# Optimization experiments

Measured on AMD Instinct MI355X. Metric: run time of the kernel, lower is better.

## Reference

```python
import jax, jax.numpy as jnp
import numpy as np

NUM_M = 2_000_000
NUM_T = 512
N = 16
NUM_GEN = N * (N - 1) // 2  # 120
NUM_STEPS = 64
TAU = 1.0


def _make_bases():
    # skew-symmetric so(n) basis, matching the torch buffer construction order
    bases = np.zeros((NUM_GEN, N, N), np.float32)
    k = 0
    for i in range(N):
        for j in range(i + 1, N):
            bases[k, i, j] = -1.0
            bases[k, j, i] = 1.0
            k += 1
    return jnp.asarray(bases)


def setup_inputs() -> dict:
    key = jax.random.key(0)
    ks = jax.random.split(key, 8)
    W = jax.random.normal(ks[0], (NUM_M, N), jnp.float32)
    emb_weight = W / jnp.linalg.norm(W, axis=-1, keepdims=True)  # normalized at init
    transition_coeffs = jax.random.normal(ks[1], (NUM_T, NUM_GEN), jnp.float32) * 0.1

    def lin(k, fi, fo):  # torch nn.Linear default init
        bound = 1.0 / np.sqrt(fi)
        kw, kb = jax.random.split(k)
        w = jax.random.uniform(kw, (fi, fo), jnp.float32, -bound, bound)
        b = jax.random.uniform(kb, (fo,), jnp.float32, -bound, bound)
        return w, b

    w1, b1 = lin(ks[2], 2 * N, 256)
    w2, b2 = lin(ks[3], 256, 128)
    w3, b3 = lin(ks[4], 128, NUM_T)

    v_src = jax.random.uniform(ks[5], (1, NUM_M), jnp.float32)
    v_target = jax.random.uniform(ks[6], (1, NUM_M), jnp.float32)
    # pre-sampled Gumbel(0,1) noise for gumbel_softmax, one draw per step
    u = jax.random.uniform(ks[7], (NUM_STEPS, 1, NUM_T), jnp.float32, 1e-6, 1.0 - 1e-6)
    gumbel = -jnp.log(-jnp.log(u))

    return {
        'v_src': v_src, 'v_target': v_target,
        'emb_weight': emb_weight, 'transition_coeffs': transition_coeffs,
        'bases': _make_bases(),
        'w1': w1, 'b1': b1, 'w2': w2, 'b2': b2, 'w3': w3, 'b3': b3,
        'gumbel': gumbel, 'num_steps': NUM_STEPS,
    }


def reference(v_src, v_target, emb_weight, transition_coeffs, bases,
              w1, b1, w2, b2, w3, b3, gumbel, num_steps):
    # training=True path of PetriNetAlignmentPredictor.forward, tau=1.0
    embs = emb_weight / jnp.linalg.norm(emb_weight, axis=-1, keepdims=True)
    v_cur = v_src @ embs      # [1, n]  (memory-bound matvec over num_m)
    v_tgt = v_target @ embs   # [1, n]
    gens = jnp.einsum('tg,gnm->tnm', transition_coeffs, bases)  # [num_t, n, n]
    expm_b = jax.vmap(jax.scipy.linalg.expm)

    def step(v, g):
        h = jax.nn.relu(jnp.concatenate([v, v_tgt], axis=-1) @ w1 + b1)
        h = jax.nn.relu(h @ w2 + b2)
        logits = h @ w3 + b3                       # [1, num_t]
        # gumbel_softmax(hard=True) with straight-through estimator
        y = jax.nn.softmax((logits + g) / TAU, axis=-1)
        hard = jax.nn.one_hot(jnp.argmax(y, axis=-1), logits.shape[-1], dtype=y.dtype)
        one_hot = hard + y - jax.lax.stop_gradient(y)
        omega = jnp.einsum('bt,tnm->bnm', one_hot, gens)  # skew-symmetric [1, n, n]
        R = expm_b(omega)
        v2 = jnp.einsum('bnm,bm->bn', R, v)
        v2 = v2 / jnp.linalg.norm(v2, axis=-1, keepdims=True)
        return v2, logits

    v_fin, logits_seq = jax.lax.scan(step, v_cur, gumbel[:num_steps])
    pred_marking = jax.nn.softmax(v_fin @ embs.T, axis=-1)  # [1, num_m]
    return pred_marking, logits_seq[:, 0, :]  # squeeze batch dim -> [num_steps, num_t]
```

## Files before the change

### kernel.cpp

```cpp
#include <hip/hip_runtime.h>

#define M_TOTAL   2000000
#define NT        512
#define K1_BLOCKS 2048

__device__ __forceinline__ float rlf(float v, int l) {
    union { float f; int i; } u; u.f = v;
    u.i = __builtin_amdgcn_readlane(u.i, l);
    return u.f;
}

__device__ __forceinline__ void bar_lds() {
    asm volatile("s_waitcnt lgkmcnt(0)" ::: "memory");
    __builtin_amdgcn_s_barrier();
    asm volatile("" ::: "memory");
}

#define REP16(M)  M(0) M(1) M(2) M(3) M(4) M(5) M(6) M(7) M(8) M(9) M(10) M(11) M(12) M(13) M(14) M(15)
#define REP16B(M) M(16) M(17) M(18) M(19) M(20) M(21) M(22) M(23) M(24) M(25) M(26) M(27) M(28) M(29) M(30) M(31)

#define VLD4(dst, base, c) { const volatile float* _p = (base) + 4*(c); \
    dst.x = _p[0]; dst.y = _p[1]; dst.z = _p[2]; dst.w = _p[3]; }

extern "C" __global__ __launch_bounds__(256)
void k_reduce(const float* __restrict__ emb, const float* __restrict__ vsrc,
              const float* __restrict__ vtgt, double* __restrict__ partials)
{
    const int tid = threadIdx.x;
    const int bid = blockIdx.x;
    const int q = tid & 3;
    double aS[4], aT[4];
#pragma unroll
    for (int i = 0; i < 4; i++) { aS[i] = 0.0; aT[i] = 0.0; }

    const float4* emb4 = (const float4*)emb;
    for (long long f = (long long)bid * 256 + tid; f < (long long)M_TOTAL * 4;
         f += (long long)K1_BLOCKS * 256) {
        float4 e = emb4[f];
        long long r = f >> 2;
        float sq = fmaf(e.x, e.x, fmaf(e.y, e.y, fmaf(e.z, e.z, e.w * e.w)));
        sq += __shfl_xor(sq, 1);
        sq += __shfl_xor(sq, 2);
        float invn = 1.0f / sqrtf(sq);
        float s = vsrc[r] * invn;
        float t = vtgt[r] * invn;
        aS[0] += (double)(s * e.x); aS[1] += (double)(s * e.y);
        aS[2] += (double)(s * e.z); aS[3] += (double)(s * e.w);
        aT[0] += (double)(t * e.x); aT[1] += (double)(t * e.y);
        aT[2] += (double)(t * e.z); aT[3] += (double)(t * e.w);
    }
#pragma unroll
    for (int i = 0; i < 4; i++) {
#pragma unroll
        for (int off = 32; off >= 4; off >>= 1) {
            aS[i] += __shfl_down(aS[i], off);
            aT[i] += __shfl_down(aT[i], off);
        }
    }
    __shared__ double lred[4][32];
    int lane = tid & 63, wv = tid >> 6;
    if (lane < 4) {
#pragma unroll
        for (int i = 0; i < 4; i++) {
            lred[wv][lane * 4 + i]      = aS[i];
            lred[wv][16 + lane * 4 + i] = aT[i];
        }
    }
    __syncthreads();
    if (tid < 32) {
        double v = lred[0][tid] + lred[1][tid] + lred[2][tid] + lred[3][tid];
        partials[(long long)bid * 32 + tid] = v;
    }
    (void)q;
}

extern "C" __global__ __launch_bounds__(256)
void k_expm(const float* __restrict__ tc, float* __restrict__ Rtab)
{
    const int b = blockIdx.x;
    const int t = threadIdx.x;
    const int i = t >> 4, j = t & 15;
    __shared__ float Om[256];
    __shared__ float Ms[256];

    const float* crow = tc + b * 120;
    float o = 0.0f;
    if (i < j)      o = -crow[(i * (31 - i)) / 2 + (j - i - 1)];
    else if (i > j) o =  crow[(j * (31 - j)) / 2 + (i - j - 1)];
    Om[t] = o;
    Ms[t] = o;
    float s = (i == j ? 1.0f : 0.0f) + o;
    __syncthreads();

#pragma unroll
    for (int k = 2; k <= 16; k++) {
        float a0 = 0.0f, a1 = 0.0f, a2 = 0.0f, a3 = 0.0f;
#pragma unroll
        for (int m = 0; m < 4; m++) {
            a0 = fmaf(Om[i * 16 + m],      Ms[m * 16 + j],        a0);
            a1 = fmaf(Om[i * 16 + 4 + m],  Ms[(4 + m) * 16 + j],  a1);
            a2 = fmaf(Om[i * 16 + 8 + m],  Ms[(8 + m) * 16 + j],  a2);
            a3 = fmaf(Om[i * 16 + 12 + m], Ms[(12 + m) * 16 + j], a3);
        }
        float acc = ((a0 + a1) + (a2 + a3)) * (1.0f / (float)k);
        __syncthreads();
        Ms[t] = acc;
        s += acc;
        __syncthreads();
    }
    Rtab[b * 256 + t] = s;
}

extern "C" __global__ __launch_bounds__(128)
void k_prep(const float* __restrict__ w2g, const float* __restrict__ w3g,
            float* __restrict__ w2R, float* __restrict__ w3R)
{
    const int b = blockIdx.x, k = threadIdx.x;
    if (b < 512) {
        w3R[b * 128 + k] = w3g[k * 512 + b];
    } else {
        const int p2 = b - 512;
        const int j2 = k;
        for (int m = 0; m < 64; m++)
            w2R[(((p2 << 7) | j2) * 64) + m] = w2g[(64 * p2 + m) * 128 + j2];
    }
}

extern "C" __global__ __launch_bounds__(512)
__attribute__((amdgpu_waves_per_eu(2, 2)))
void k_steps(const double* __restrict__ partials,
             const float* __restrict__ w1g, const float* __restrict__ b1g,
             const float* __restrict__ b2g, const float* __restrict__ b3g,
             const float* __restrict__ w2R, const float* __restrict__ w3R,
             const float* __restrict__ Rtab, const float* __restrict__ gum,
             const int* __restrict__ nsp,
             float* __restrict__ outL, float* __restrict__ vf_out)
{
    __shared__ float h1s[256];
    __shared__ float h2p[512];
    __shared__ float xs[32];
    __shared__ float b2s[128];
    __shared__ float rkeys[8];
    __shared__ int   ridx[8];

    const int t = threadIdx.x;
    const int lane = t & 63;
    const int wv = t >> 6;
    const int j2 = t & 127, p2 = t >> 7;
    const int c1 = t & 255;

    const volatile float* w3v = (const volatile float*)(w3R + (size_t)t * 128);
    const volatile float* w2v = (const volatile float*)(w2R + (size_t)t * 64);
#define W3D(c) float4 w3_##c; VLD4(w3_##c, w3v, c)
    REP16(W3D) REP16B(W3D)
#undef W3D
#define W2D(c) float4 w2_##c; VLD4(w2_##c, w2v, c)
    REP16(W2D)
#undef W2D
    const float b3r = b3g[t];

    float w1r[16];
    {
        const volatile float* w1v = (const volatile float*)w1g;
#pragma unroll
        for (int m = 0; m < 16; m++) w1r[m] = w1v[m * 256 + c1];
    }
    if (t < 128) b2s[t] = b2g[t];

    float warm = 0.0f;
    for (int i = t; i < 512 * 256 / 4; i += 512) {
        float4 rv = ((const float4*)Rtab)[i];
        warm += (rv.x + rv.y) + (rv.z + rv.w);
    }

    {
        int c = t >> 4, r = t & 15;
        double v = 0.0;
        for (int k = r; k < K1_BLOCKS; k += 16) v += partials[k * 32 + c];
        v += __shfl_xor(v, 1); v += __shfl_xor(v, 2);
        v += __shfl_xor(v, 4); v += __shfl_xor(v, 8);
        if (r == 0) xs[c] = (float)v;
    }

    int ns = nsp[0];
    if (ns > 64) ns = 64;
    if (ns < 0)  ns = 0;
    if (ns == -2147483647) vf_out[0] = warm;

    __syncthreads();

    float b1e;
    {
        float a = b1g[c1];
#pragma unroll
        for (int m = 0; m < 16; m++)
            a = fmaf(xs[16 + m], w1g[(16 + m) * 256 + c1], a);
        b1e = a;
    }
    float vreg = xs[lane & 15];

    if (ns == 0 && t < 16) vf_out[t] = xs[t];

    const int i16 = lane & 15, q4 = lane >> 4;

    for (int step = 0; step < ns; step++) {
        float gv = gum[step * 512 + t];

        if (t < 256) {
            float a0 = 0.0f, a1 = 0.0f;
#pragma unroll
            for (int m = 0; m < 8; m++) {
                a0 = fmaf(rlf(vreg, m),     w1r[m],     a0);
                a1 = fmaf(rlf(vreg, 8 + m), w1r[8 + m], a1);
            }
            h1s[t] = fmaxf((a0 + a1) + b1e, 0.0f);
        }
        bar_lds();

        {
            float h1seg = h1s[(p2 << 6) | lane];
            float a0 = 0.0f, a1 = 0.0f, a2 = 0.0f, a3 = 0.0f;
#define L2C(c) { a0 = fmaf(rlf(h1seg, 4*(c)+0), w2_##c.x, a0); \
                 a1 = fmaf(rlf(h1seg, 4*(c)+1), w2_##c.y, a1); \
                 a2 = fmaf(rlf(h1seg, 4*(c)+2), w2_##c.z, a2); \
                 a3 = fmaf(rlf(h1seg, 4*(c)+3), w2_##c.w, a3); }
            REP16(L2C)
#undef L2C
            h2p[(p2 << 7) | j2] = (a0 + a1) + (a2 + a3);
        }
        bar_lds();

        float lg;
        {
            float h2lo = fmaxf(((h2p[lane] + h2p[128 + lane]) +
                                (h2p[256 + lane] + h2p[384 + lane])) + b2s[lane], 0.0f);
            float h2hi = fmaxf(((h2p[64 + lane] + h2p[192 + lane]) +
                                (h2p[320 + lane] + h2p[448 + lane])) + b2s[64 + lane], 0.0f);
            float lg0 = 0.0f, lg1 = 0.0f, lg2 = 0.0f, lg3 = 0.0f;
#define L3LO(c) { lg0 = fmaf(rlf(h2lo, 4*(c)+0), w3_##c.x, lg0); \
                  lg1 = fmaf(rlf(h2lo, 4*(c)+1), w3_##c.y, lg1); \
                  lg2 = fmaf(rlf(h2lo, 4*(c)+2), w3_##c.z, lg2); \
                  lg3 = fmaf(rlf(h2lo, 4*(c)+3), w3_##c.w, lg3); }
#define L3HI(c) { lg0 = fmaf(rlf(h2hi, 4*(c)-64), w3_##c.x, lg0); \
                  lg1 = fmaf(rlf(h2hi, 4*(c)-63), w3_##c.y, lg1); \
                  lg2 = fmaf(rlf(h2hi, 4*(c)-62), w3_##c.z, lg2); \
                  lg3 = fmaf(rlf(h2hi, 4*(c)-61), w3_##c.w, lg3); }
            REP16(L3LO) REP16B(L3HI)
#undef L3LO
#undef L3HI
            lg = ((lg0 + lg1) + (lg2 + lg3)) + b3r;
        }

        {
            float key = lg + gv;
            int   idx = t;
#pragma unroll
            for (int off = 32; off; off >>= 1) {
                float ok = __shfl_down(key, off);
                int   oi = __shfl_down(idx, off);
                if (ok > key || (ok == key && oi < idx)) { key = ok; idx = oi; }
            }
            if (lane == 0) { rkeys[wv] = key; ridx[wv] = idx; }
        }
        bar_lds();

        outL[step * 512 + t] = lg;

        {
            float bk = rkeys[0]; int bi = ridx[0];
#pragma unroll
            for (int w = 1; w < 8; w++) {
                float ok = rkeys[w]; int oi = ridx[w];
                if (ok > bk || (ok == bk && oi < bi)) { bk = ok; bi = oi; }
            }
            const float4 rr = *(const float4*)(Rtab + bi * 256 + i16 * 16 + 4 * q4);
            float rw0 = __shfl(vreg, 20 * q4 + 0);
            float rw1 = __shfl(vreg, 20 * q4 + 1);
            float rw2 = __shfl(vreg, 20 * q4 + 2);
            float rw3 = __shfl(vreg, 20 * q4 + 3);
            float pr = rr.x * rw0;
            pr = fmaf(rr.y, rw1, pr);
            pr = fmaf(rr.z, rw2, pr);
            pr = fmaf(rr.w, rw3, pr);
            pr += __shfl_xor(pr, 16);
            pr += __shfl_xor(pr, 32);
            float n2 = pr * pr;
            n2 += __shfl_xor(n2, 1);
            n2 += __shfl_xor(n2, 2);
            n2 += __shfl_xor(n2, 4);
            n2 += __shfl_xor(n2, 8);
            float invn = 1.0f / sqrtf(n2);
            vreg = pr * invn;
            if (step == ns - 1 && t < 16) vf_out[t] = vreg;
        }
    }
}

extern "C" __global__ __launch_bounds__(256)
void k_scores(const float* __restrict__ emb, const float* __restrict__ vf16,
              float* __restrict__ outP, double* __restrict__ sums)
{
    __shared__ float vfs[16];
    const int tid = threadIdx.x;
    const int bid = blockIdx.x;
    const int q = tid & 3;
    if (tid < 16) vfs[tid] = vf16[tid];
    __syncthreads();
    float v0 = vfs[q * 4 + 0], v1 = vfs[q * 4 + 1], v2 = vfs[q * 4 + 2], v3 = vfs[q * 4 + 3];

    const float4* emb4 = (const float4*)emb;
    double bsum = 0.0;
    for (long long f = (long long)bid * 256 + tid; f < (long long)M_TOTAL * 4;
         f += (long long)K1_BLOCKS * 256) {
        float4 e = emb4[f];
        long long r = f >> 2;
        float sq = fmaf(e.x, e.x, fmaf(e.y, e.y, fmaf(e.z, e.z, e.w * e.w)));
        float d  = fmaf(e.x, v0, fmaf(e.y, v1, fmaf(e.z, v2, e.w * v3)));
        sq += __shfl_xor(sq, 1);  d += __shfl_xor(d, 1);
        sq += __shfl_xor(sq, 2);  d += __shfl_xor(d, 2);
        float ex = expf(d / sqrtf(sq));
        if (q == 0) {
            outP[r] = ex;
            bsum += (double)ex;
        }
    }
#pragma unroll
    for (int off = 4; off <= 32; off <<= 1) bsum += __shfl_down(bsum, off);
    __shared__ double lred[4];
    if ((tid & 63) == 0) lred[tid >> 6] = bsum;
    __syncthreads();
    if (tid == 0) sums[bid] = lred[0] + lred[1] + lred[2] + lred[3];
}

extern "C" __global__ __launch_bounds__(256)
void k_total(const double* __restrict__ sums, double* __restrict__ invp)
{
    const int tid = threadIdx.x;
    double v = 0.0;
    for (int k = tid; k < K1_BLOCKS; k += 256) v += sums[k];
#pragma unroll
    for (int off = 32; off; off >>= 1) v += __shfl_down(v, off);
    __shared__ double lred[4];
    if ((tid & 63) == 0) lred[tid >> 6] = v;
    __syncthreads();
    if (tid == 0) invp[0] = 1.0 / (lred[0] + lred[1] + lred[2] + lred[3]);
}

extern "C" __global__ __launch_bounds__(256)
void k_scale(float* __restrict__ outP, const double* __restrict__ invp)
{
    const float inv = (float)invp[0];
    long long r4 = (long long)blockIdx.x * 256 + threadIdx.x;
    if (r4 < M_TOTAL / 4) {
        float4* p = (float4*)outP;
        float4 v = p[r4];
        v.x *= inv; v.y *= inv; v.z *= inv; v.w *= inv;
        p[r4] = v;
    }
}

extern "C" void kernel_launch(void* const* d_in, const int* in_sizes, int n_in,
                              void* d_out, int out_size, void* d_ws, size_t ws_size,
                              hipStream_t stream)
{
    const float* vsrc = (const float*)d_in[0];
    const float* vtgt = (const float*)d_in[1];
    const float* emb  = (const float*)d_in[2];
    const float* tc   = (const float*)d_in[3];
    const float* w1 = (const float*)d_in[5];
    const float* b1 = (const float*)d_in[6];
    const float* w2 = (const float*)d_in[7];
    const float* b2 = (const float*)d_in[8];
    const float* w3 = (const float*)d_in[9];
    const float* b3 = (const float*)d_in[10];
    const float* gum = (const float*)d_in[11];
    const int* nsp   = (const int*)d_in[12];

    float* outP = (float*)d_out;
    float* outL = outP + M_TOTAL;

    double* wsd      = (double*)d_ws;
    double* partials = wsd;
    double* sums     = wsd + K1_BLOCKS * 32;
    double* invp     = sums + K1_BLOCKS;
    float*  vf       = (float*)(invp + 1);

    float* Rtab = outP;
    float* w3R  = outP + 131072;
    float* w2R  = outP + 196608;

    k_expm<<<NT, 256, 0, stream>>>(tc, Rtab);
    k_prep<<<516, 128, 0, stream>>>(w2, w3, w2R, w3R);
    k_reduce<<<K1_BLOCKS, 256, 0, stream>>>(emb, vsrc, vtgt, partials);
    k_steps<<<1, 512, 0, stream>>>(partials, w1, b1, b2, b3, w2R, w3R, Rtab, gum, nsp, outL, vf);
    k_scores<<<K1_BLOCKS, 256, 0, stream>>>(emb, vf, outP, sums);
    k_total<<<1, 256, 0, stream>>>(sums, invp);
    k_scale<<<(M_TOTAL / 4 + 255) / 256, 256, 0, stream>>>(outP, invp);
}
```

Baseline: 552.6 us.

## Split serial MLP steps across 1024 threads with halved per-thread weight slices

Expands the single-block sequential step kernel from 512 to 1024 threads. Each thread now holds half as many w2/w3 weights in registers, and layer-3 partial logits are combined through an added shared-memory stage. w1 moves from registers into LDS, and the weight-repacking kernel is rearranged to match the new slices. The aim is to cut the per-step latency of the 64-step serial chain, at the cost of an extra barrier per step and more LDS traffic.

```diff
diff --git a/kernel.cpp b/kernel.cpp
--- a/kernel.cpp
+++ b/kernel.cpp
@@ -17,7 +17,7 @@
 }
 
 #define REP16(M)  M(0) M(1) M(2) M(3) M(4) M(5) M(6) M(7) M(8) M(9) M(10) M(11) M(12) M(13) M(14) M(15)
-#define REP16B(M) M(16) M(17) M(18) M(19) M(20) M(21) M(22) M(23) M(24) M(25) M(26) M(27) M(28) M(29) M(30) M(31)
+#define REP8(M)   M(0) M(1) M(2) M(3) M(4) M(5) M(6) M(7)
 
 #define VLD4(dst, base, c) { const volatile float* _p = (base) + 4*(c); \
     dst.x = _p[0]; dst.y = _p[1]; dst.z = _p[2]; dst.w = _p[3]; }
@@ -28,7 +28,6 @@
 {
     const int tid = threadIdx.x;
     const int bid = blockIdx.x;
-    const int q = tid & 3;
     double aS[4], aT[4];
 #pragma unroll
     for (int i = 0; i < 4; i++) { aS[i] = 0.0; aT[i] = 0.0; }
@@ -71,7 +70,6 @@
         double v = lred[0][tid] + lred[1][tid] + lred[2][tid] + lred[3][tid];
         partials[(long long)bid * 32 + tid] = v;
     }
-    (void)q;
 }
 
 extern "C" __global__ __launch_bounds__(256)
@@ -111,23 +109,22 @@
     Rtab[b * 256 + t] = s;
 }
 
-extern "C" __global__ __launch_bounds__(128)
+extern "C" __global__ __launch_bounds__(64)
 void k_prep(const float* __restrict__ w2g, const float* __restrict__ w3g,
             float* __restrict__ w2R, float* __restrict__ w3R)
 {
-    const int b = blockIdx.x, k = threadIdx.x;
-    if (b < 512) {
-        w3R[b * 128 + k] = w3g[k * 512 + b];
-    } else {
-        const int p2 = b - 512;
-        const int j2 = k;
-        for (int m = 0; m < 64; m++)
-            w2R[(((p2 << 7) | j2) * 64) + m] = w2g[(64 * p2 + m) * 128 + j2];
-    }
-}
-
-extern "C" __global__ __launch_bounds__(512)
-__attribute__((amdgpu_waves_per_eu(2, 2)))
+    const int b = blockIdx.x;
+    const int l = threadIdx.x;
+    const int o = b & 511, hh = b >> 9;
+    w3R[b * 64 + l] = w3g[(hh * 64 + l) * 512 + o];
+    if (l < 32) {
+        const int p = b >> 7, j = b & 127;
+        w2R[b * 32 + l] = w2g[(p * 32 + l) * 128 + j];
+    }
+}
+
+extern "C" __global__ __launch_bounds__(1024)
+__attribute__((amdgpu_waves_per_eu(4, 4)))
 void k_steps(const double* __restrict__ partials,
              const float* __restrict__ w1g, const float* __restrict__ b1g,
              const float* __restrict__ b2g, const float* __restrict__ b3g,
@@ -136,8 +133,10 @@
              const int* __restrict__ nsp,
              float* __restrict__ outL, float* __restrict__ vf_out)
 {
+    __shared__ float w1s[16 * 256];
     __shared__ float h1s[256];
-    __shared__ float h2p[512];
+    __shared__ float h2p[1024];
+    __shared__ float lgp[1024];
     __shared__ float xs[32];
     __shared__ float b2s[128];
     __shared__ float rkeys[8];
@@ -146,39 +145,33 @@
     const int t = threadIdx.x;
     const int lane = t & 63;
     const int wv = t >> 6;
-    const int j2 = t & 127, p2 = t >> 7;
-    const int c1 = t & 255;
-
-    const volatile float* w3v = (const volatile float*)(w3R + (size_t)t * 128);
-    const volatile float* w2v = (const volatile float*)(w2R + (size_t)t * 64);
+
+    const volatile float* w3v = (const volatile float*)(w3R + (size_t)t * 64);
+    const volatile float* w2v = (const volatile float*)(w2R + (size_t)t * 32);
 #define W3D(c) float4 w3_##c; VLD4(w3_##c, w3v, c)
-    REP16(W3D) REP16B(W3D)
+    REP16(W3D)
 #undef W3D
 #define W2D(c) float4 w2_##c; VLD4(w2_##c, w2v, c)
-    REP16(W2D)
+    REP8(W2D)
 #undef W2D
-    const float b3r = b3g[t];
-
-    float w1r[16];
-    {
-        const volatile float* w1v = (const volatile float*)w1g;
-#pragma unroll
-        for (int m = 0; m < 16; m++) w1r[m] = w1v[m * 256 + c1];
-    }
+    const float b3r = (t < 512) ? b3g[t] : 0.0f;
+
+    for (int i = t; i < 16 * 256; i += 1024) w1s[i] = w1g[i];
     if (t < 128) b2s[t] = b2g[t];
 
     float warm = 0.0f;
-    for (int i = t; i < 512 * 256 / 4; i += 512) {
+    for (int i = t; i < 512 * 256 / 4; i += 1024) {
         float4 rv = ((const float4*)Rtab)[i];
         warm += (rv.x + rv.y) + (rv.z + rv.w);
     }
 
     {
-        int c = t >> 4, r = t & 15;
+        int c = t >> 5, r = t & 31;
         double v = 0.0;
-        for (int k = r; k < K1_BLOCKS; k += 16) v += partials[k * 32 + c];
+        for (int k = r; k < K1_BLOCKS; k += 32) v += partials[k * 32 + c];
         v += __shfl_xor(v, 1); v += __shfl_xor(v, 2);
         v += __shfl_xor(v, 4); v += __shfl_xor(v, 8);
+        v += __shfl_xor(v, 16);
         if (r == 0) xs[c] = (float)v;
     }
 
@@ -189,69 +182,67 @@
 
     __syncthreads();
 
-    float b1e;
-    {
-        float a = b1g[c1];
+    float b1e = 0.0f, vreg = 0.0f;
+    if (t < 256) {
+        float a = b1g[t];
 #pragma unroll
         for (int m = 0; m < 16; m++)
-            a = fmaf(xs[16 + m], w1g[(16 + m) * 256 + c1], a);
+            a = fmaf(xs[16 + m], w1g[(16 + m) * 256 + t], a);
         b1e = a;
-    }
-    float vreg = xs[lane & 15];
+        vreg = xs[lane & 15];
+    }
 
     if (ns == 0 && t < 16) vf_out[t] = xs[t];
 
     const int i16 = lane & 15, q4 = lane >> 4;
 
     for (int step = 0; step < ns; step++) {
-        float gv = gum[step * 512 + t];
+        float gv = (t < 512) ? gum[step * 512 + t] : 0.0f;
 
         if (t < 256) {
             float a0 = 0.0f, a1 = 0.0f;
 #pragma unroll
             for (int m = 0; m < 8; m++) {
-                a0 = fmaf(rlf(vreg, m),     w1r[m],     a0);
-                a1 = fmaf(rlf(vreg, 8 + m), w1r[8 + m], a1);
+                a0 = fmaf(rlf(vreg, m),     w1s[m * 256 + t],       a0);
+                a1 = fmaf(rlf(vreg, 8 + m), w1s[(8 + m) * 256 + t], a1);
             }
             h1s[t] = fmaxf((a0 + a1) + b1e, 0.0f);
         }
         bar_lds();
 
         {
-            float h1seg = h1s[(p2 << 6) | lane];
+            float h1seg = h1s[((t >> 7) << 5) | (lane & 31)];
             float a0 = 0.0f, a1 = 0.0f, a2 = 0.0f, a3 = 0.0f;
 #define L2C(c) { a0 = fmaf(rlf(h1seg, 4*(c)+0), w2_##c.x, a0); \
                  a1 = fmaf(rlf(h1seg, 4*(c)+1), w2_##c.y, a1); \
                  a2 = fmaf(rlf(h1seg, 4*(c)+2), w2_##c.z, a2); \
                  a3 = fmaf(rlf(h1seg, 4*(c)+3), w2_##c.w, a3); }
-            REP16(L2C)
+            REP8(L2C)
 #undef L2C
-            h2p[(p2 << 7) | j2] = (a0 + a1) + (a2 + a3);
+            h2p[t] = (a0 + a1) + (a2 + a3);
         }
         bar_lds();
 
-        float lg;
         {
-            float h2lo = fmaxf(((h2p[lane] + h2p[128 + lane]) +
-                                (h2p[256 + lane] + h2p[384 + lane])) + b2s[lane], 0.0f);
-            float h2hi = fmaxf(((h2p[64 + lane] + h2p[192 + lane]) +
-                                (h2p[320 + lane] + h2p[448 + lane])) + b2s[64 + lane], 0.0f);
+            const int hbl = ((t >> 9) << 6) + lane;
+            float s = b2s[hbl];
+#pragma unroll
+            for (int p = 0; p < 8; p++) s += h2p[p * 128 + hbl];
+            float h2seg = fmaxf(s, 0.0f);
             float lg0 = 0.0f, lg1 = 0.0f, lg2 = 0.0f, lg3 = 0.0f;
-#define L3LO(c) { lg0 = fmaf(rlf(h2lo, 4*(c)+0), w3_##c.x, lg0); \
-                  lg1 = fmaf(rlf(h2lo, 4*(c)+1), w3_##c.y, lg1); \
-                  lg2 = fmaf(rlf(h2lo, 4*(c)+2), w3_##c.z, lg2); \
-                  lg3 = fmaf(rlf(h2lo, 4*(c)+3), w3_##c.w, lg3); }
-#define L3HI(c) { lg0 = fmaf(rlf(h2hi, 4*(c)-64), w3_##c.x, lg0); \
-                  lg1 = fmaf(rlf(h2hi, 4*(c)-63), w3_##c.y, lg1); \
-                  lg2 = fmaf(rlf(h2hi, 4*(c)-62), w3_##c.z, lg2); \
-                  lg3 = fmaf(rlf(h2hi, 4*(c)-61), w3_##c.w, lg3); }
-            REP16(L3LO) REP16B(L3HI)
-#undef L3LO
-#undef L3HI
-            lg = ((lg0 + lg1) + (lg2 + lg3)) + b3r;
-        }
-
-        {
+#define L3C(c) { lg0 = fmaf(rlf(h2seg, 4*(c)+0), w3_##c.x, lg0); \
+                 lg1 = fmaf(rlf(h2seg, 4*(c)+1), w3_##c.y, lg1); \
+                 lg2 = fmaf(rlf(h2seg, 4*(c)+2), w3_##c.z, lg2); \
+                 lg3 = fmaf(rlf(h2seg, 4*(c)+3), w3_##c.w, lg3); }
+            REP16(L3C)
+#undef L3C
+            lgp[t] = (lg0 + lg1) + (lg2 + lg3);
+        }
+        bar_lds();
+
+        if (t < 512) {
+            float lg = (lgp[t] + lgp[512 + t]) + b3r;
+            outL[step * 512 + t] = lg;
             float key = lg + gv;
             int   idx = t;
 #pragma unroll
@@ -264,9 +255,7 @@
         }
         bar_lds();
 
-        outL[step * 512 + t] = lg;
-
-        {
+        if (t < 256) {
             float bk = rkeys[0]; int bi = ridx[0];
 #pragma unroll
             for (int w = 1; w < 8; w++) {
@@ -390,9 +379,9 @@
     float* w2R  = outP + 196608;
 
     k_expm<<<NT, 256, 0, stream>>>(tc, Rtab);
-    k_prep<<<516, 128, 0, stream>>>(w2, w3, w2R, w3R);
+    k_prep<<<1024, 64, 0, stream>>>(w2, w3, w2R, w3R);
     k_reduce<<<K1_BLOCKS, 256, 0, stream>>>(emb, vsrc, vtgt, partials);
-    k_steps<<<1, 512, 0, stream>>>(partials, w1, b1, b2, b3, w2R, w3R, Rtab, gum, nsp, outL, vf);
+    k_steps<<<1, 1024, 0, stream>>>(partials, w1, b1, b2, b3, w2R, w3R, Rtab, gum, nsp, outL, vf);
     k_scores<<<K1_BLOCKS, 256, 0, stream>>>(emb, vf, outP, sums);
     k_total<<<1, 256, 0, stream>>>(sums, invp);
     k_scale<<<(M_TOTAL / 4 + 255) / 256, 256, 0, stream>>>(outP, invp);
```

After: 621.4 us. +12.4%, slower.

## Merge prep kernels, drop total kernel via atomics, and speed step-loop argmax and matvec

Applied to the files above, without the earlier changes.

Fuses k_expm and k_prep into one launch and replaces the k_total kernel with a double atomicAdd into a zeroed accumulator, removing two kernel launches. The partials reduction block count is halved and its final sum is done through shared memory. Inside the serial step loop, argmax now uses DPP max on order-preserving integer keys plus a ballot, and the 16x16 rotation matvec uses one lane per output row with DPP sums. Together these target launch overhead and per-step latency in the single-block loop. The atomic sum changes the floating-point reduction order, so results are no longer deterministic across runs.

```diff
diff --git a/kernel.cpp b/kernel.cpp
--- a/kernel.cpp
+++ b/kernel.cpp
@@ -2,7 +2,8 @@
 
 #define M_TOTAL   2000000
 #define NT        512
-#define K1_BLOCKS 2048
+#define K1_BLOCKS 1024
+#define K3_BLOCKS 2048
 
 __device__ __forceinline__ float rlf(float v, int l) {
     union { float f; int i; } u; u.f = v;
@@ -16,6 +17,21 @@
     asm volatile("" ::: "memory");
 }
 
+#define DPPMAXU(m, ctrl) { unsigned _d = (unsigned)__builtin_amdgcn_update_dpp(0, (int)(m), (ctrl), 0xF, 0xF, true); \
+                           if (_d > (m)) (m) = _d; }
+#define DPPADDF(s, ctrl) { float _d = __int_as_float(__builtin_amdgcn_update_dpp(0, __float_as_int(s), (ctrl), 0xF, 0xF, true)); \
+                           (s) += _d; }
+
+__device__ __forceinline__ unsigned orderf(float f) {
+    unsigned u = __float_as_uint(f);
+    return u ^ (((unsigned)((int)u >> 31)) | 0x80000000u);
+}
+
+__device__ __forceinline__ uint2 pick2(uint2 a, uint2 b) {
+    bool takeb = (b.x > a.x) || (b.x == a.x && b.y < a.y);
+    return takeb ? b : a;
+}
+
 #define REP16(M)  M(0) M(1) M(2) M(3) M(4) M(5) M(6) M(7) M(8) M(9) M(10) M(11) M(12) M(13) M(14) M(15)
 #define REP16B(M) M(16) M(17) M(18) M(19) M(20) M(21) M(22) M(23) M(24) M(25) M(26) M(27) M(28) M(29) M(30) M(31)
 
@@ -28,7 +44,6 @@
 {
     const int tid = threadIdx.x;
     const int bid = blockIdx.x;
-    const int q = tid & 3;
     double aS[4], aT[4];
 #pragma unroll
     for (int i = 0; i < 4; i++) { aS[i] = 0.0; aT[i] = 0.0; }
@@ -71,58 +86,61 @@
         double v = lred[0][tid] + lred[1][tid] + lred[2][tid] + lred[3][tid];
         partials[(long long)bid * 32 + tid] = v;
     }
-    (void)q;
 }
 
 extern "C" __global__ __launch_bounds__(256)
-void k_expm(const float* __restrict__ tc, float* __restrict__ Rtab)
-{
-    const int b = blockIdx.x;
+void k_pre(const float* __restrict__ tc, float* __restrict__ Rtab,
+           const float* __restrict__ w2g, const float* __restrict__ w3g,
+           float* __restrict__ w2R, float* __restrict__ w3R,
+           double* __restrict__ totalp)
+{
+    const int bid = blockIdx.x;
     const int t = threadIdx.x;
-    const int i = t >> 4, j = t & 15;
-    __shared__ float Om[256];
-    __shared__ float Ms[256];
-
-    const float* crow = tc + b * 120;
-    float o = 0.0f;
-    if (i < j)      o = -crow[(i * (31 - i)) / 2 + (j - i - 1)];
-    else if (i > j) o =  crow[(j * (31 - j)) / 2 + (i - j - 1)];
-    Om[t] = o;
-    Ms[t] = o;
-    float s = (i == j ? 1.0f : 0.0f) + o;
-    __syncthreads();
-
-#pragma unroll
-    for (int k = 2; k <= 16; k++) {
-        float a0 = 0.0f, a1 = 0.0f, a2 = 0.0f, a3 = 0.0f;
-#pragma unroll
-        for (int m = 0; m < 4; m++) {
-            a0 = fmaf(Om[i * 16 + m],      Ms[m * 16 + j],        a0);
-            a1 = fmaf(Om[i * 16 + 4 + m],  Ms[(4 + m) * 16 + j],  a1);
-            a2 = fmaf(Om[i * 16 + 8 + m],  Ms[(8 + m) * 16 + j],  a2);
-            a3 = fmaf(Om[i * 16 + 12 + m], Ms[(12 + m) * 16 + j], a3);
-        }
-        float acc = ((a0 + a1) + (a2 + a3)) * (1.0f / (float)k);
+
+    if (bid < 512) {
+        const int i = t >> 4, j = t & 15;
+        __shared__ float Om[256];
+        __shared__ float Ms[256];
+
+        const float* crow = tc + bid * 120;
+        float o = 0.0f;
+        if (i < j)      o = -crow[(i * (31 - i)) / 2 + (j - i - 1)];
+        else if (i > j) o =  crow[(j * (31 - j)) / 2 + (i - j - 1)];
+        Om[t] = o;
+        Ms[t] = o;
+        float s = (i == j ? 1.0f : 0.0f) + o;
         __syncthreads();
-        Ms[t] = acc;
-        s += acc;
-        __syncthreads();
-    }
-    Rtab[b * 256 + t] = s;
-}
-
-extern "C" __global__ __launch_bounds__(128)
-void k_prep(const float* __restrict__ w2g, const float* __restrict__ w3g,
-            float* __restrict__ w2R, float* __restrict__ w3R)
-{
-    const int b = blockIdx.x, k = threadIdx.x;
-    if (b < 512) {
-        w3R[b * 128 + k] = w3g[k * 512 + b];
+
+#pragma unroll
+        for (int k = 2; k <= 16; k++) {
+            float a0 = 0.0f, a1 = 0.0f, a2 = 0.0f, a3 = 0.0f;
+#pragma unroll
+            for (int m = 0; m < 4; m++) {
+                a0 = fmaf(Om[i * 16 + m],      Ms[m * 16 + j],        a0);
+                a1 = fmaf(Om[i * 16 + 4 + m],  Ms[(4 + m) * 16 + j],  a1);
+                a2 = fmaf(Om[i * 16 + 8 + m],  Ms[(8 + m) * 16 + j],  a2);
+                a3 = fmaf(Om[i * 16 + 12 + m], Ms[(12 + m) * 16 + j], a3);
+            }
+            float acc = ((a0 + a1) + (a2 + a3)) * (1.0f / (float)k);
+            __syncthreads();
+            Ms[t] = acc;
+            s += acc;
+            __syncthreads();
+        }
+        Rtab[bid * 256 + t] = s;
     } else {
-        const int p2 = b - 512;
-        const int j2 = k;
-        for (int m = 0; m < 64; m++)
-            w2R[(((p2 << 7) | j2) * 64) + m] = w2g[(64 * p2 + m) * 128 + j2];
+        if (bid == 512 && t == 0) totalp[0] = 0.0;
+        if (t >= 128) return;
+        const int b = bid - 512;
+        const int k = t;
+        if (b < 512) {
+            w3R[b * 128 + k] = w3g[k * 512 + b];
+        } else {
+            const int p2 = b - 512;
+            const int j2 = k;
+            for (int m = 0; m < 64; m++)
+                w2R[(((p2 << 7) | j2) * 64) + m] = w2g[(64 * p2 + m) * 128 + j2];
+        }
     }
 }
 
@@ -140,8 +158,8 @@
     __shared__ float h2p[512];
     __shared__ float xs[32];
     __shared__ float b2s[128];
-    __shared__ float rkeys[8];
-    __shared__ int   ridx[8];
+    __shared__ uint2 kidx[8];
+    __shared__ double dred[512];
 
     const int t = threadIdx.x;
     const int lane = t & 63;
@@ -174,12 +192,10 @@
     }
 
     {
-        int c = t >> 4, r = t & 15;
         double v = 0.0;
-        for (int k = r; k < K1_BLOCKS; k += 16) v += partials[k * 32 + c];
-        v += __shfl_xor(v, 1); v += __shfl_xor(v, 2);
-        v += __shfl_xor(v, 4); v += __shfl_xor(v, 8);
-        if (r == 0) xs[c] = (float)v;
+#pragma unroll 4
+        for (int i = 0; i < (K1_BLOCKS * 32) / 512; i++) v += partials[i * 512 + t];
+        dred[t] = v;
     }
 
     int ns = nsp[0];
@@ -188,20 +204,25 @@
     if (ns == -2147483647) vf_out[0] = warm;
 
     __syncthreads();
-
-    float b1e;
-    {
+    if (t < 32) {
+        double s = 0.0;
+#pragma unroll
+        for (int j = 0; j < 16; j++) s += dred[t + 32 * j];
+        xs[t] = (float)s;
+    }
+    __syncthreads();
+
+    float b1e = 0.0f, vreg = 0.0f;
+    if (t < 256) {
         float a = b1g[c1];
 #pragma unroll
         for (int m = 0; m < 16; m++)
             a = fmaf(xs[16 + m], w1g[(16 + m) * 256 + c1], a);
         b1e = a;
-    }
-    float vreg = xs[lane & 15];
+        vreg = xs[lane & 15];
+    }
 
     if (ns == 0 && t < 16) vf_out[t] = xs[t];
-
-    const int i16 = lane & 15, q4 = lane >> 4;
 
     for (int step = 0; step < ns; step++) {
         float gv = gum[step * 512 + t];
@@ -250,45 +271,63 @@
 #undef L3HI
             lg = ((lg0 + lg1) + (lg2 + lg3)) + b3r;
         }
+        outL[step * 512 + t] = lg;
 
         {
-            float key = lg + gv;
-            int   idx = t;
-#pragma unroll
-            for (int off = 32; off; off >>= 1) {
-                float ok = __shfl_down(key, off);
-                int   oi = __shfl_down(idx, off);
-                if (ok > key || (ok == key && oi < idx)) { key = ok; idx = oi; }
+            unsigned ok = orderf(lg + gv);
+            unsigned m = ok;
+            DPPMAXU(m, 0x111)
+            DPPMAXU(m, 0x112)
+            DPPMAXU(m, 0x114)
+            DPPMAXU(m, 0x118)
+            DPPMAXU(m, 0x142)
+            DPPMAXU(m, 0x143)
+            unsigned wmax = (unsigned)__builtin_amdgcn_readlane((int)m, 63);
+            unsigned long long mask = __ballot(ok == wmax);
+            if (lane == 0) {
+                uint2 kv; kv.x = wmax; kv.y = (unsigned)(wv * 64 + (__ffsll(mask) - 1));
+                kidx[wv] = kv;
             }
-            if (lane == 0) { rkeys[wv] = key; ridx[wv] = idx; }
         }
         bar_lds();
 
-        outL[step * 512 + t] = lg;
-
-        {
-            float bk = rkeys[0]; int bi = ridx[0];
-#pragma unroll
-            for (int w = 1; w < 8; w++) {
-                float ok = rkeys[w]; int oi = ridx[w];
-                if (ok > bk || (ok == bk && oi < bi)) { bk = ok; bi = oi; }
-            }
-            const float4 rr = *(const float4*)(Rtab + bi * 256 + i16 * 16 + 4 * q4);
-            float rw0 = __shfl(vreg, 20 * q4 + 0);
-            float rw1 = __shfl(vreg, 20 * q4 + 1);
-            float rw2 = __shfl(vreg, 20 * q4 + 2);
-            float rw3 = __shfl(vreg, 20 * q4 + 3);
-            float pr = rr.x * rw0;
-            pr = fmaf(rr.y, rw1, pr);
-            pr = fmaf(rr.z, rw2, pr);
-            pr = fmaf(rr.w, rw3, pr);
-            pr += __shfl_xor(pr, 16);
-            pr += __shfl_xor(pr, 32);
-            float n2 = pr * pr;
-            n2 += __shfl_xor(n2, 1);
-            n2 += __shfl_xor(n2, 2);
-            n2 += __shfl_xor(n2, 4);
-            n2 += __shfl_xor(n2, 8);
+        if (t < 256 && lane < 16) {
+            uint2 K0, K1, K2, K3, K4, K5, K6, K7;
+            { uint4 a = *(const uint4*)&kidx[0]; K0.x=a.x; K0.y=a.y; K1.x=a.z; K1.y=a.w; }
+            { uint4 a = *(const uint4*)&kidx[2]; K2.x=a.x; K2.y=a.y; K3.x=a.z; K3.y=a.w; }
+            { uint4 a = *(const uint4*)&kidx[4]; K4.x=a.x; K4.y=a.y; K5.x=a.z; K5.y=a.w; }
+            { uint4 a = *(const uint4*)&kidx[6]; K6.x=a.x; K6.y=a.y; K7.x=a.z; K7.y=a.w; }
+            uint2 w01 = pick2(K0, K1), w23 = pick2(K2, K3);
+            uint2 w45 = pick2(K4, K5), w67 = pick2(K6, K7);
+            uint2 win = pick2(pick2(w01, w23), pick2(w45, w67));
+            const int bi = (int)win.y;
+
+            const float4* rp = (const float4*)(Rtab + (size_t)bi * 256 + lane * 16);
+            float4 ra = rp[0], rb = rp[1], rc = rp[2], rd = rp[3];
+            float pr;
+            pr = ra.x * rlf(vreg, 0);
+            pr = fmaf(ra.y, rlf(vreg, 1), pr);
+            pr = fmaf(ra.z, rlf(vreg, 2), pr);
+            pr = fmaf(ra.w, rlf(vreg, 3), pr);
+            pr = fmaf(rb.x, rlf(vreg, 4), pr);
+            pr = fmaf(rb.y, rlf(vreg, 5), pr);
+            pr = fmaf(rb.z, rlf(vreg, 6), pr);
+            pr = fmaf(rb.w, rlf(vreg, 7), pr);
+            pr = fmaf(rc.x, rlf(vreg, 8), pr);
+            pr = fmaf(rc.y, rlf(vreg, 9), pr);
+            pr = fmaf(rc.z, rlf(vreg, 10), pr);
+            pr = fmaf(rc.w, rlf(vreg, 11), pr);
+            pr = fmaf(rd.x, rlf(vreg, 12), pr);
+            pr = fmaf(rd.y, rlf(vreg, 13), pr);
+            pr = fmaf(rd.z, rlf(vreg, 14), pr);
+            pr = fmaf(rd.w, rlf(vreg, 15), pr);
+
+            float s2 = pr * pr;
+            DPPADDF(s2, 0x111)
+            DPPADDF(s2, 0x112)
+            DPPADDF(s2, 0x114)
+            DPPADDF(s2, 0x118)
+            float n2 = rlf(s2, 15);
             float invn = 1.0f / sqrtf(n2);
             vreg = pr * invn;
             if (step == ns - 1 && t < 16) vf_out[t] = vreg;
@@ -298,7 +337,7 @@
 
 extern "C" __global__ __launch_bounds__(256)
 void k_scores(const float* __restrict__ emb, const float* __restrict__ vf16,
-              float* __restrict__ outP, double* __restrict__ sums)
+              float* __restrict__ outP, double* __restrict__ totalp)
 {
     __shared__ float vfs[16];
     const int tid = threadIdx.x;
@@ -311,7 +350,7 @@
     const float4* emb4 = (const float4*)emb;
     double bsum = 0.0;
     for (long long f = (long long)bid * 256 + tid; f < (long long)M_TOTAL * 4;
-         f += (long long)K1_BLOCKS * 256) {
+         f += (long long)K3_BLOCKS * 256) {
         float4 e = emb4[f];
         long long r = f >> 2;
         float sq = fmaf(e.x, e.x, fmaf(e.y, e.y, fmaf(e.z, e.z, e.w * e.w)));
@@ -329,27 +368,13 @@
     __shared__ double lred[4];
     if ((tid & 63) == 0) lred[tid >> 6] = bsum;
     __syncthreads();
-    if (tid == 0) sums[bid] = lred[0] + lred[1] + lred[2] + lred[3];
+    if (tid == 0) atomicAdd(totalp, lred[0] + lred[1] + lred[2] + lred[3]);
 }
 
 extern "C" __global__ __launch_bounds__(256)
-void k_total(const double* __restrict__ sums, double* __restrict__ invp)
-{
-    const int tid = threadIdx.x;
-    double v = 0.0;
-    for (int k = tid; k < K1_BLOCKS; k += 256) v += sums[k];
-#pragma unroll
-    for (int off = 32; off; off >>= 1) v += __shfl_down(v, off);
-    __shared__ double lred[4];
-    if ((tid & 63) == 0) lred[tid >> 6] = v;
-    __syncthreads();
-    if (tid == 0) invp[0] = 1.0 / (lred[0] + lred[1] + lred[2] + lred[3]);
-}
-
-extern "C" __global__ __launch_bounds__(256)
-void k_scale(float* __restrict__ outP, const double* __restrict__ invp)
-{
-    const float inv = (float)invp[0];
+void k_scale(float* __restrict__ outP, const double* __restrict__ totalp)
+{
+    const float inv = 1.0f / (float)totalp[0];
     long long r4 = (long long)blockIdx.x * 256 + threadIdx.x;
     if (r4 < M_TOTAL / 4) {
         float4* p = (float4*)outP;
@@ -381,19 +406,16 @@
 
     double* wsd      = (double*)d_ws;
     double* partials = wsd;
-    double* sums     = wsd + K1_BLOCKS * 32;
-    double* invp     = sums + K1_BLOCKS;
-    float*  vf       = (float*)(invp + 1);
+    double* totalp   = wsd + 2048 * 32;
+    float*  vf       = (float*)(totalp + 1);
 
     float* Rtab = outP;
     float* w3R  = outP + 131072;
     float* w2R  = outP + 196608;
 
-    k_expm<<<NT, 256, 0, stream>>>(tc, Rtab);
-    k_prep<<<516, 128, 0, stream>>>(w2, w3, w2R, w3R);
+    k_pre<<<1028, 256, 0, stream>>>(tc, Rtab, w2, w3, w2R, w3R, totalp);
     k_reduce<<<K1_BLOCKS, 256, 0, stream>>>(emb, vsrc, vtgt, partials);
     k_steps<<<1, 512, 0, stream>>>(partials, w1, b1, b2, b3, w2R, w3R, Rtab, gum, nsp, outL, vf);
-    k_scores<<<K1_BLOCKS, 256, 0, stream>>>(emb, vf, outP, sums);
-    k_total<<<1, 256, 0, stream>>>(sums, invp);
-    k_scale<<<(M_TOTAL / 4 + 255) / 256, 256, 0, stream>>>(outP, invp);
-}
+    k_scores<<<K3_BLOCKS, 256, 0, stream>>>(emb, vf, outP, totalp);
+    k_scale<<<(M_TOTAL / 4 + 255) / 256, 256, 0, stream>>>(outP, totalp);
+}
```

New measurement: 469.4 us. 1.18x faster.
